# Optimization experiments

Measured on AMD Instinct MI355X. Metric: run time of the kernel, lower is better.

## Reference

```python
import jax, jax.numpy as jnp
import numpy as np

# dims: H heads, D=word_size (d_model), E=embed_dim per head, N=seq_len=n, K=linformer k
H, D, E, N, K = 16, 1024, 64, 4096, 256


def setup_inputs() -> dict:
    key = jax.random.key(0)
    ks = jax.random.split(key, 9)
    s = 0.02  # init scale for weights
    return {
        "x":  jax.random.normal(ks[0], (N, D), jnp.float32),
        # per-head QKV linears: torch Linear weight is (out=E, in=D), bias (E,)
        "Wq": jax.random.normal(ks[1], (H, E, D), jnp.float32) * s,
        "bq": jnp.zeros((H, E), jnp.float32),
        "Wk": jax.random.normal(ks[2], (H, E, D), jnp.float32) * s,
        "bk": jnp.zeros((H, E), jnp.float32),
        "Wv": jax.random.normal(ks[3], (H, E, D), jnp.float32) * s,
        "bv": jnp.zeros((H, E), jnp.float32),
        # per-head E/F sequence projections: Linear(n=N, k=K) -> weight (K, N), bias (K,)
        "Ew": jax.random.normal(ks[4], (H, K, N), jnp.float32) * s,
        "Eb": jnp.zeros((H, K), jnp.float32),
        "Fw": jax.random.normal(ks[5], (H, K, N), jnp.float32) * s,
        "Fb": jnp.zeros((H, K), jnp.float32),
        # output projection: Linear(H*E, E, bias=False) -> weight (E, H*E)
        "Wo": jax.random.normal(ks[6], (E, H * E), jnp.float32) * s,
    }


def reference(x, Wq, bq, Wk, bk, Wv, bv, Ew, Eb, Fw, Fb, Wo):
    # per-head Q/K/V projections, batched over heads: (H, N, E)
    q = jnp.einsum('nd,hed->hne', x, Wq) + bq[:, None, :]
    k = jnp.einsum('nd,hed->hne', x, Wk) + bk[:, None, :]
    v = jnp.einsum('nd,hed->hne', x, Wv) + bv[:, None, :]
    # low-rank sequence-length projection of K and V: (H, K, E)
    kp = jnp.einsum('hjn,hne->hje', Ew, k) + Eb[:, :, None]
    vp = jnp.einsum('hjn,hne->hje', Fw, v) + Fb[:, :, None]
    # scaled dot-product attention against projected keys: (H, N, K)
    score = jnp.einsum('hne,hje->hnj', q, kp) / jnp.sqrt(jnp.float32(E))
    attn = jax.nn.softmax(score, axis=-1)
    z = jnp.einsum('hnj,hje->hne', attn, vp)  # (H, N, E)
    # concat heads along feature dim (matches torch.cat(dim=1)): (N, H*E)
    zs = jnp.transpose(z, (1, 0, 2)).reshape(N, H * E)
    # final projection Linear(H*E, E, bias=False)
    return zs @ Wo.T  # (N, E)
```

## Files before the change

kernel.cpp:

```cpp
#include <hip/hip_runtime.h>
#include <hip/hip_bf16.h>

typedef __attribute__((ext_vector_type(4))) float f32x4;
typedef __attribute__((ext_vector_type(8))) short s16x8;
typedef __attribute__((ext_vector_type(4))) short s16x4;
typedef unsigned short u16;


__device__ __forceinline__ f32x4 mfma16(s16x8 a, s16x8 b, f32x4 c) {
    return __builtin_amdgcn_mfma_f32_16x16x32_bf16(a, b, c, 0, 0, 0);
}

__device__ __forceinline__ u16 bf(float f) {
    union { float f; unsigned u; } x; x.f = f;
    return (u16)((x.u + 0x7fffu + ((x.u >> 16) & 1u)) >> 16);
}
__device__ __forceinline__ unsigned pkbf(float a, float b) {
    union { float f; unsigned u; } x, y; x.f = a; y.f = b;
    unsigned ra = x.u + 0x7fffu + ((x.u >> 16) & 1u);
    unsigned rb = y.u + 0x7fffu + ((y.u >> 16) & 1u);
    return (ra >> 16) | (rb & 0xffff0000u);
}

__device__ __forceinline__ void gl_lds16(const u16* g, u16* l) {
    __builtin_amdgcn_global_load_lds(
        (const __attribute__((address_space(1))) unsigned*)g,
        (__attribute__((address_space(3))) unsigned*)l, 16, 0, 0);
}


__global__ __launch_bounds__(256) void cvt_all_kernel(
        const float* __restrict__ x,  const float* __restrict__ Wq,
        const float* __restrict__ Wk, const float* __restrict__ Wv,
        const float* __restrict__ Wo,
        u16* __restrict__ xb, u16* __restrict__ wb, u16* __restrict__ wob) {
    int i = blockIdx.x * 256 + threadIdx.x;
    const float* src; u16* dst; int off;
    if (i < 1048576)      { src = x;  dst = xb;            off = i; }
    else if (i < 1310720) { src = Wq; dst = wb;            off = i - 1048576; }
    else if (i < 1572864) { src = Wk; dst = wb + 1048576;  off = i - 1310720; }
    else if (i < 1835008) { src = Wv; dst = wb + 2097152;  off = i - 1572864; }
    else if (i < 1851392) { src = Wo; dst = wob;           off = i - 1835008; }
    else return;
    f32x4 v = ((const f32x4*)src)[off];
    union { s16x4 v; unsigned u[2]; } r;
    r.u[0] = pkbf(v.x, v.y);
    r.u[1] = pkbf(v.z, v.w);
    ((s16x4*)dst)[off] = r.v;
}


__global__ __launch_bounds__(256, 3) void qkv_kernel(
        const u16* __restrict__ xb, const u16* __restrict__ wb,
        const float* __restrict__ bq, const float* __restrict__ bk,
        const float* __restrict__ bv,
        u16* __restrict__ qo, u16* __restrict__ kTo, u16* __restrict__ vTo) {
    __shared__ u16 As[128 * 32];
    __shared__ u16 Bs[128 * 32];
    int bx   = blockIdx.x % 24;
    int by   = blockIdx.x / 24;
    int tid  = threadIdx.x;
    int lane = tid & 63, w = tid >> 6;
    int l15  = lane & 15, quad = lane >> 4;
    int wr   = w >> 1, wc = w & 1;

    const u16* Ag = xb + (size_t)(by * 128 + (tid >> 2)) * 1024 + (tid & 3) * 8;
    const u16* Bg = wb + (size_t)(bx * 128 + (tid >> 2)) * 1024 + (tid & 3) * 8;
    u16* Al = As + tid * 8;
    u16* Bl = Bs + tid * 8;

    const u16* abase = As + (wr * 64 + l15) * 32 + quad * 8;
    const u16* bbase = Bs + (wc * 64 + l15) * 32 + quad * 8;

    f32x4 acc[4][4] = {};
    for (int k0 = 0; k0 < 1024; k0 += 32) {
        gl_lds16(Ag + k0, Al);
        gl_lds16(Ag + 64 * 1024 + k0, Al + 64 * 32);
        gl_lds16(Bg + k0, Bl);
        gl_lds16(Bg + 64 * 1024 + k0, Bl + 64 * 32);
        __syncthreads();
        s16x8 a[4], b[4];
#pragma unroll
        for (int mi = 0; mi < 4; mi++) a[mi] = *(const s16x8*)(abase + mi * 16 * 32);
#pragma unroll
        for (int nj = 0; nj < 4; nj++) b[nj] = *(const s16x8*)(bbase + nj * 16 * 32);
#pragma unroll
        for (int mi = 0; mi < 4; mi++)
#pragma unroll
            for (int nj = 0; nj < 4; nj++) acc[mi][nj] = mfma16(a[mi], b[nj], acc[mi][nj]);
        __syncthreads();
    }

    int fblk = (bx * 128 + wc * 64) >> 6;
    int mat  = fblk >> 4, h = fblk & 15;
    const float* bias = (mat == 0) ? bq : (mat == 1 ? bk : bv);
#pragma unroll
    for (int nj = 0; nj < 4; nj++) {
        int e = nj * 16 + l15;
        float bb = bias[h * 64 + e];
#pragma unroll
        for (int mi = 0; mi < 4; mi++) {
            int n0 = by * 128 + wr * 64 + mi * 16 + quad * 4;
            f32x4 c = acc[mi][nj];
            if (mat == 0) {
                u16* p = qo + ((size_t)h * 4096 + n0) * 64 + e;
#pragma unroll
                for (int r = 0; r < 4; r++) p[(size_t)r * 64] = bf(c[r] + bb);
            } else {
                u16* p = (mat == 1 ? kTo : vTo) + ((size_t)h * 64 + e) * 4096 + n0;
                union { s16x4 v; u16 s[4]; } pk;
#pragma unroll
                for (int r = 0; r < 4; r++) pk.s[r] = bf(c[r] + bb);
                *(s16x4*)p = pk.v;
            }
        }
    }
}


__global__ __launch_bounds__(256, 2) void kpvp_kernel(
        const float* __restrict__ Ew, const float* __restrict__ Fw,
        const u16* __restrict__ kT, const u16* __restrict__ vT,
        float* __restrict__ accs) {
    __shared__ u16 As[256 * 40];
    __shared__ u16 Bs[64 * 32];
    int b    = blockIdx.x;
    int ks   = b & 15, h = (b >> 4) & 15, p = b >> 8;
    int tid  = threadIdx.x;
    int lane = tid & 63, w = tid >> 6;
    int l15  = lane & 15, quad = lane >> 4;

    const float* Ag = (p ? Fw : Ew)
        + (size_t)(h * 256 + (tid >> 3)) * 4096 + ks * 256 + (tid & 7) * 4;
    const u16* Bg = (p ? vT : kT)
        + ((size_t)h * 64 + (tid >> 2)) * 4096 + ks * 256 + (tid & 3) * 8;
    u16* Aw = As + (tid >> 3) * 40 + (tid & 7) * 4;
    u16* Bl = Bs + tid * 8;

    const u16* abase = As + (w * 64 + l15) * 40 + quad * 8;
    const u16* bbase = Bs + l15 * 32 + quad * 8;

    f32x4 acc[4][4] = {};
    for (int s = 0; s < 8; s++) {
        int kk = s * 32;
        gl_lds16(Bg + kk, Bl);
#pragma unroll
        for (int pr = 0; pr < 8; pr++) {
            f32x4 v = *(const f32x4*)(Ag + (size_t)pr * 32 * 4096 + kk);
            union { s16x4 q; unsigned u[2]; } rr;
            rr.u[0] = pkbf(v.x, v.y);
            rr.u[1] = pkbf(v.z, v.w);
            *(s16x4*)(Aw + pr * 32 * 40) = rr.q;
        }
        __syncthreads();
        s16x8 a[4], bb2[4];
#pragma unroll
        for (int mt = 0; mt < 4; mt++) a[mt] = *(const s16x8*)(abase + mt * 16 * 40);
#pragma unroll
        for (int nt = 0; nt < 4; nt++) bb2[nt] = *(const s16x8*)(bbase + nt * 16 * 32);
#pragma unroll
        for (int mt = 0; mt < 4; mt++)
#pragma unroll
            for (int nt = 0; nt < 4; nt++)
                acc[mt][nt] = mfma16(a[mt], bb2[nt], acc[mt][nt]);
        __syncthreads();
    }

    size_t base = (size_t)ks * 524288
        + ((size_t)(p * 16 + h) * 256 + w * 64 + quad * 4) * 64 + l15;
#pragma unroll
    for (int mt = 0; mt < 4; mt++)
#pragma unroll
        for (int nt = 0; nt < 4; nt++)
#pragma unroll
            for (int r = 0; r < 4; r++)
                accs[base + (size_t)(mt * 16 + r) * 64 + nt * 16] = acc[mt][nt][r];
}


__global__ __launch_bounds__(256) void packkv_kernel(
        const float* __restrict__ accs, const float* __restrict__ Eb,
        const float* __restrict__ Fb, u16* __restrict__ kp, u16* __restrict__ vpT) {
    int idx = blockIdx.x * 256 + threadIdx.x;
    float v = 0.f;
#pragma unroll
    for (int s = 0; s < 16; s++) v += accs[idx + (size_t)s * 524288];
    int p = idx >> 18, h = (idx >> 14) & 15, j = (idx >> 6) & 255, e = idx & 63;
    if (p == 0) {
        v += Eb[h * 256 + j];
        kp[((size_t)(h * 256 + j)) * 64 + e] = bf(v * 0.125f);
    } else {
        v += Fb[h * 256 + j];
        vpT[((size_t)(h * 64 + e)) * 256 + j] = bf(v);
    }
}


__global__ __launch_bounds__(256) void attn_kernel(
        const u16* __restrict__ q, const u16* __restrict__ kp,
        const u16* __restrict__ vpT, u16* __restrict__ zs) {
    __shared__ u16 ps[4][16][256];
    int bm   = blockIdx.x & 63, h = blockIdx.x >> 6;
    int lane = threadIdx.x & 63, w = threadIdx.x >> 6;
    int l15  = lane & 15, quad = lane >> 4;
    int nbase = bm * 64 + w * 16;

    f32x4 s[16] = {};
    const u16* qp  = q  + ((size_t)h * 4096 + nbase + l15) * 64 + quad * 8;
    const u16* kpp = kp + ((size_t)h * 256 + l15) * 64 + quad * 8;
#pragma unroll
    for (int e0 = 0; e0 < 64; e0 += 32) {
        s16x8 a = *(const s16x8*)(qp + e0);
#pragma unroll
        for (int jt = 0; jt < 16; jt++) {
            s16x8 b = *(const s16x8*)(kpp + jt * 16 * 64 + e0);
            s[jt] = mfma16(a, b, s[jt]);
        }
    }

    float lsum[4];
#pragma unroll
    for (int r = 0; r < 4; r++) {
        float m = s[0][r];
#pragma unroll
        for (int jt = 1; jt < 16; jt++) m = fmaxf(m, s[jt][r]);
        m = fmaxf(m, __shfl_xor(m, 1));
        m = fmaxf(m, __shfl_xor(m, 2));
        m = fmaxf(m, __shfl_xor(m, 4));
        m = fmaxf(m, __shfl_xor(m, 8));
        float l = 0.f;
#pragma unroll
        for (int jt = 0; jt < 16; jt++) {
            float pv = __expf(s[jt][r] - m);
            s[jt][r] = pv;
            l += pv;
        }
        l += __shfl_xor(l, 1);
        l += __shfl_xor(l, 2);
        l += __shfl_xor(l, 4);
        l += __shfl_xor(l, 8);
        lsum[r] = l;
    }

#pragma unroll
    for (int jt = 0; jt < 16; jt++)
#pragma unroll
        for (int r = 0; r < 4; r++)
            ps[w][quad * 4 + r][jt * 16 + l15] = bf(s[jt][r]);
    __syncthreads();

    f32x4 z[4] = {};
    const u16* vp = vpT + ((size_t)h * 64 + l15) * 256 + quad * 8;
#pragma unroll
    for (int kj = 0; kj < 8; kj++) {
        s16x8 a = *(const s16x8*)&ps[w][l15][kj * 32 + quad * 8];
#pragma unroll
        for (int et = 0; et < 4; et++) {
            s16x8 b = *(const s16x8*)(vp + et * 16 * 256 + kj * 32);
            z[et] = mfma16(a, b, z[et]);
        }
    }
#pragma unroll
    for (int et = 0; et < 4; et++) {
        int e = et * 16 + l15;
        u16* o = zs + ((size_t)(nbase + quad * 4)) * 1024 + h * 64 + e;
#pragma unroll
        for (int r = 0; r < 4; r++) o[(size_t)r * 1024] = bf(z[et][r] / lsum[r]);
    }
}


__global__ __launch_bounds__(256) void out_kernel(
        const u16* __restrict__ zs, const u16* __restrict__ wob,
        float* __restrict__ oslice) {
    int ks   = blockIdx.x & 3;
    int bm   = blockIdx.x >> 2;
    int lane = threadIdx.x & 63, w = threadIdx.x >> 6;
    int l15  = lane & 15, quad = lane >> 4;
    int row0 = bm * 128 + w * 32;

    const u16* A = zs  + (size_t)(row0 + l15) * 1024 + ks * 256 + quad * 8;
    const u16* B = wob + (size_t)l15 * 1024 + ks * 256 + quad * 8;

    f32x4 acc[2][4] = {};
    for (int k = 0; k < 256; k += 32) {
        s16x8 a0 = *(const s16x8*)(A + k);
        s16x8 a1 = *(const s16x8*)(A + 16 * 1024 + k);
#pragma unroll
        for (int nt = 0; nt < 4; nt++) {
            s16x8 bv = *(const s16x8*)(B + (size_t)nt * 16 * 1024 + k);
            acc[0][nt] = mfma16(a0, bv, acc[0][nt]);
            acc[1][nt] = mfma16(a1, bv, acc[1][nt]);
        }
    }
    float* os = oslice + (size_t)ks * 262144;
#pragma unroll
    for (int mt = 0; mt < 2; mt++)
#pragma unroll
        for (int nt = 0; nt < 4; nt++) {
            int e = nt * 16 + l15;
            int n0 = row0 + mt * 16 + quad * 4;
            float* o = os + (size_t)n0 * 64 + e;
#pragma unroll
            for (int r = 0; r < 4; r++) o[(size_t)r * 64] = acc[mt][nt][r];
        }
}

__global__ __launch_bounds__(256) void outred_kernel(
        const float* __restrict__ oslice, float* __restrict__ out) {
    int i = blockIdx.x * 256 + threadIdx.x;
    out[i] = oslice[i] + oslice[i + 262144] + oslice[i + 524288] + oslice[i + 786432];
}


extern "C" void kernel_launch(void* const* d_in, const int* in_sizes, int n_in,
                              void* d_out, int out_size, void* d_ws, size_t ws_size,
                              hipStream_t stream) {
    const float* x  = (const float*)d_in[0];
    const float* Wq = (const float*)d_in[1];
    const float* bq = (const float*)d_in[2];
    const float* Wk = (const float*)d_in[3];
    const float* bk = (const float*)d_in[4];
    const float* Wv = (const float*)d_in[5];
    const float* bv = (const float*)d_in[6];
    const float* Ew = (const float*)d_in[7];
    const float* Eb = (const float*)d_in[8];
    const float* Fw = (const float*)d_in[9];
    const float* Fb = (const float*)d_in[10];
    const float* Wo = (const float*)d_in[11];

    char* ws = (char*)d_ws;
    u16*   qb   = (u16*)(ws + 0);
    u16*   kT   = (u16*)(ws + 8388608);
    u16*   vT   = (u16*)(ws + 16777216);
    u16*   zsb  = (u16*)(ws + 25165824);
    float* accs = (float*)(ws + 33554432);
    u16*   kp   = (u16*)(ws + 67108864);
    u16*   vpT  = (u16*)(ws + 67633152);
    u16*   xb   = (u16*)(ws + 68157440);
    u16*   wb   = (u16*)(ws + 76546048);
    u16*   wob  = (u16*)(ws + 82837504);

    cvt_all_kernel<<<7232, 256, 0, stream>>>(x, Wq, Wk, Wv, Wo, xb, wb, wob);
    qkv_kernel<<<768, 256, 0, stream>>>(xb, wb, bq, bk, bv, qb, kT, vT);
    kpvp_kernel<<<512, 256, 0, stream>>>(Ew, Fw, kT, vT, accs);
    packkv_kernel<<<2048, 256, 0, stream>>>(accs, Eb, Fb, kp, vpT);
    attn_kernel<<<1024, 256, 0, stream>>>(qb, kp, vpT, zsb);
    out_kernel<<<128, 256, 0, stream>>>(zsb, wob, (float*)accs);
    outred_kernel<<<1024, 256, 0, stream>>>((const float*)accs, (float*)d_out);
}
```

Measured before the change: 300.4 us.

## Retile kpvp split-K and stage attention K/V projections in swizzled LDS

Measured after the change: 264.2 us. -12.0%, faster.

```diff
diff --git a/kernel.cpp b/kernel.cpp
--- a/kernel.cpp
+++ b/kernel.cpp
@@ -22,7 +22,7 @@
     return (ra >> 16) | (rb & 0xffff0000u);
 }
 
-__device__ __forceinline__ void gl_lds16(const u16* g, u16* l) {
+__device__ __forceinline__ void gl_lds16(const void* g, void* l) {
     __builtin_amdgcn_global_load_lds(
         (const __attribute__((address_space(1))) unsigned*)g,
         (__attribute__((address_space(3))) unsigned*)l, 16, 0, 0);
@@ -118,63 +118,79 @@
 }
 
 
-__global__ __launch_bounds__(256, 2) void kpvp_kernel(
+__global__ __launch_bounds__(512, 2) void kpvp_kernel(
         const float* __restrict__ Ew, const float* __restrict__ Fw,
         const u16* __restrict__ kT, const u16* __restrict__ vT,
         float* __restrict__ accs) {
-    __shared__ u16 As[256 * 40];
-    __shared__ u16 Bs[64 * 32];
-    int b    = blockIdx.x;
-    int ks   = b & 15, h = (b >> 4) & 15, p = b >> 8;
-    int tid  = threadIdx.x;
-    int lane = tid & 63, w = tid >> 6;
-    int l15  = lane & 15, quad = lane >> 4;
-
-    const float* Ag = (p ? Fw : Ew)
-        + (size_t)(h * 256 + (tid >> 3)) * 4096 + ks * 256 + (tid & 7) * 4;
-    const u16* Bg = (p ? vT : kT)
-        + ((size_t)h * 64 + (tid >> 2)) * 4096 + ks * 256 + (tid & 3) * 8;
-    u16* Aw = As + (tid >> 3) * 40 + (tid & 7) * 4;
-    u16* Bl = Bs + tid * 8;
-
-    const u16* abase = As + (w * 64 + l15) * 40 + quad * 8;
-    const u16* bbase = Bs + l15 * 32 + quad * 8;
-
-    f32x4 acc[4][4] = {};
+    __shared__ u16 Als[64 * 256];
+    __shared__ u16 Bls[64 * 256];
+    int b   = blockIdx.x;
+    int ks  = b & 1, jb = (b >> 1) & 3, h = (b >> 3) & 15, p = b >> 7;
+    int tid = threadIdx.x;
+    int w = tid >> 6, lane = tid & 63;
+    int l15 = lane & 15, quad = lane >> 4;
+    int wm = w >> 2, we = w & 3;
+
+    const float* Abase = (p ? Fw : Ew)
+        + (size_t)(h * 256 + jb * 64) * 4096 + ks * 2048;
+    const char* Bbase = (const char*)(p ? vT : kT)
+        + (size_t)h * 64 * 8192 + ks * 4096;
+
+    f32x4 areg[8];
+#pragma unroll
+    for (int pr = 0; pr < 8; pr++)
+        areg[pr] = *(const f32x4*)(Abase + (size_t)(pr * 8 + w) * 4096 + lane * 4);
+
+    f32x4 acc[2] = {};
+
+#pragma unroll
     for (int s = 0; s < 8; s++) {
-        int kk = s * 32;
-        gl_lds16(Bg + kk, Bl);
+        __syncthreads();
+#pragma unroll
+        for (int i = 0; i < 4; i++) {
+            int row = (w * 4 + i) * 2 + (lane >> 5);
+            int c   = lane & 31;
+            int cg  = (c & 24) | ((c & 7) ^ (row & 7));
+            gl_lds16(Bbase + (size_t)row * 8192 + s * 512 + cg * 16,
+                     (char*)Bls + (w * 4 + i) * 1024);
+        }
 #pragma unroll
         for (int pr = 0; pr < 8; pr++) {
-            f32x4 v = *(const f32x4*)(Ag + (size_t)pr * 32 * 4096 + kk);
+            int row = pr * 8 + w;
             union { s16x4 q; unsigned u[2]; } rr;
-            rr.u[0] = pkbf(v.x, v.y);
-            rr.u[1] = pkbf(v.z, v.w);
-            *(s16x4*)(Aw + pr * 32 * 40) = rr.q;
+            rr.u[0] = pkbf(areg[pr].x, areg[pr].y);
+            rr.u[1] = pkbf(areg[pr].z, areg[pr].w);
+            int c  = lane >> 1;
+            int cw = (c & 24) | ((c & 7) ^ (w & 7));
+            *(s16x4*)((char*)Als + row * 512 + cw * 16 + (lane & 1) * 8) = rr.q;
         }
         __syncthreads();
-        s16x8 a[4], bb2[4];
-#pragma unroll
-        for (int mt = 0; mt < 4; mt++) a[mt] = *(const s16x8*)(abase + mt * 16 * 40);
-#pragma unroll
-        for (int nt = 0; nt < 4; nt++) bb2[nt] = *(const s16x8*)(bbase + nt * 16 * 32);
-#pragma unroll
-        for (int mt = 0; mt < 4; mt++)
-#pragma unroll
-            for (int nt = 0; nt < 4; nt++)
-                acc[mt][nt] = mfma16(a[mt], bb2[nt], acc[mt][nt]);
-        __syncthreads();
-    }
-
-    size_t base = (size_t)ks * 524288
-        + ((size_t)(p * 16 + h) * 256 + w * 64 + quad * 4) * 64 + l15;
-#pragma unroll
-    for (int mt = 0; mt < 4; mt++)
-#pragma unroll
-        for (int nt = 0; nt < 4; nt++)
-#pragma unroll
-            for (int r = 0; r < 4; r++)
-                accs[base + (size_t)(mt * 16 + r) * 64 + nt * 16] = acc[mt][nt][r];
+        if (s < 7) {
+#pragma unroll
+            for (int pr = 0; pr < 8; pr++)
+                areg[pr] = *(const f32x4*)(Abase + (size_t)(pr * 8 + w) * 4096
+                                           + (s + 1) * 256 + lane * 4);
+        }
+#pragma unroll
+        for (int t = 0; t < 8; t++) {
+            int c  = 4 * t + quad;
+            int ca = (c & 24) | ((c & 7) ^ (l15 & 7));
+            s16x8 bv = *(const s16x8*)((char*)Bls + (we * 16 + l15) * 512 + ca * 16);
+            s16x8 a0 = *(const s16x8*)((char*)Als + (wm * 32 + l15) * 512 + ca * 16);
+            s16x8 a1 = *(const s16x8*)((char*)Als + (wm * 32 + 16 + l15) * 512 + ca * 16);
+            acc[0] = mfma16(a0, bv, acc[0]);
+            acc[1] = mfma16(a1, bv, acc[1]);
+        }
+    }
+
+    size_t obase = (size_t)ks * 524288 + ((size_t)(p * 16 + h) * 256 + jb * 64) * 64;
+#pragma unroll
+    for (int mt = 0; mt < 2; mt++)
+#pragma unroll
+        for (int r = 0; r < 4; r++) {
+            int jrow = wm * 32 + mt * 16 + quad * 4 + r;
+            accs[obase + (size_t)jrow * 64 + we * 16 + l15] = acc[mt][r];
+        }
 }
 
 
@@ -182,9 +198,7 @@
         const float* __restrict__ accs, const float* __restrict__ Eb,
         const float* __restrict__ Fb, u16* __restrict__ kp, u16* __restrict__ vpT) {
     int idx = blockIdx.x * 256 + threadIdx.x;
-    float v = 0.f;
-#pragma unroll
-    for (int s = 0; s < 16; s++) v += accs[idx + (size_t)s * 524288];
+    float v = accs[idx] + accs[idx + 524288];
     int p = idx >> 18, h = (idx >> 14) & 15, j = (idx >> 6) & 255, e = idx & 63;
     if (p == 0) {
         v += Eb[h * 256 + j];
@@ -196,26 +210,42 @@
 }
 
 
-__global__ __launch_bounds__(256) void attn_kernel(
+__global__ __launch_bounds__(256, 2) void attn_kernel(
         const u16* __restrict__ q, const u16* __restrict__ kp,
         const u16* __restrict__ vpT, u16* __restrict__ zs) {
+    __shared__ u16 kv[16384];
     __shared__ u16 ps[4][16][256];
     int bm   = blockIdx.x & 63, h = blockIdx.x >> 6;
-    int lane = threadIdx.x & 63, w = threadIdx.x >> 6;
+    int tid  = threadIdx.x;
+    int lane = tid & 63, w = tid >> 6;
     int l15  = lane & 15, quad = lane >> 4;
     int nbase = bm * 64 + w * 16;
 
+    {
+        int r8 = lane >> 3;
+        int cg = (lane & 7) ^ r8;
+        const u16* src = kp + (size_t)h * 16384;
+#pragma unroll
+        for (int it = 0; it < 8; it++) {
+            int row = it * 32 + w * 8 + r8;
+            gl_lds16(src + row * 64 + cg * 8, (char*)kv + it * 4096 + w * 1024);
+        }
+    }
+    const u16* qp = q + ((size_t)h * 4096 + nbase + l15) * 64 + quad * 8;
+    s16x8 qa0 = *(const s16x8*)(qp);
+    s16x8 qa1 = *(const s16x8*)(qp + 32);
+    __syncthreads();
+
     f32x4 s[16] = {};
-    const u16* qp  = q  + ((size_t)h * 4096 + nbase + l15) * 64 + quad * 8;
-    const u16* kpp = kp + ((size_t)h * 256 + l15) * 64 + quad * 8;
-#pragma unroll
-    for (int e0 = 0; e0 < 64; e0 += 32) {
-        s16x8 a = *(const s16x8*)(qp + e0);
-#pragma unroll
-        for (int jt = 0; jt < 16; jt++) {
-            s16x8 b = *(const s16x8*)(kpp + jt * 16 * 64 + e0);
-            s[jt] = mfma16(a, b, s[jt]);
-        }
+#pragma unroll
+    for (int jt = 0; jt < 16; jt++) {
+        int c0 = quad ^ (l15 & 7);
+        int c1 = (quad + 4) ^ (l15 & 7);
+        const char* rowp = (const char*)kv + (jt * 16 + l15) * 128;
+        s16x8 b0 = *(const s16x8*)(rowp + c0 * 16);
+        s16x8 b1 = *(const s16x8*)(rowp + c1 * 16);
+        s[jt] = mfma16(qa0, b0, s[jt]);
+        s[jt] = mfma16(qa1, b1, s[jt]);
     }
 
     float lsum[4];
@@ -242,22 +272,37 @@
         lsum[r] = l;
     }
 
+    __syncthreads();
+    {
+        int r2 = lane >> 5;
+        int c  = lane & 31;
+        const u16* src = vpT + (size_t)h * 16384;
+#pragma unroll
+        for (int it = 0; it < 8; it++) {
+            int row = it * 8 + w * 2 + r2;
+            int cg  = (c & 24) | ((c & 7) ^ (row & 7));
+            gl_lds16(src + row * 256 + cg * 8, (char*)kv + it * 4096 + w * 1024);
+        }
+    }
 #pragma unroll
     for (int jt = 0; jt < 16; jt++)
 #pragma unroll
-        for (int r = 0; r < 4; r++)
-            ps[w][quad * 4 + r][jt * 16 + l15] = bf(s[jt][r]);
+        for (int r = 0; r < 4; r++) {
+            int row = quad * 4 + r;
+            ps[w][row][(jt * 16 + l15) ^ ((row & 7) << 3)] = bf(s[jt][r]);
+        }
     __syncthreads();
 
     f32x4 z[4] = {};
-    const u16* vp = vpT + ((size_t)h * 64 + l15) * 256 + quad * 8;
 #pragma unroll
     for (int kj = 0; kj < 8; kj++) {
-        s16x8 a = *(const s16x8*)&ps[w][l15][kj * 32 + quad * 8];
+        s16x8 a = *(const s16x8*)&ps[w][l15][(kj * 32 + quad * 8) ^ ((l15 & 7) << 3)];
 #pragma unroll
         for (int et = 0; et < 4; et++) {
-            s16x8 b = *(const s16x8*)(vp + et * 16 * 256 + kj * 32);
-            z[et] = mfma16(a, b, z[et]);
+            int c  = kj * 4 + quad;
+            int cs = (c & 24) | ((c & 7) ^ (l15 & 7));
+            s16x8 bv = *(const s16x8*)((char*)kv + (et * 16 + l15) * 512 + cs * 16);
+            z[et] = mfma16(a, bv, z[et]);
         }
     }
 #pragma unroll
@@ -343,7 +388,7 @@
 
     cvt_all_kernel<<<7232, 256, 0, stream>>>(x, Wq, Wk, Wv, Wo, xb, wb, wob);
     qkv_kernel<<<768, 256, 0, stream>>>(xb, wb, bq, bk, bv, qb, kT, vT);
-    kpvp_kernel<<<512, 256, 0, stream>>>(Ew, Fw, kT, vT, accs);
+    kpvp_kernel<<<256, 512, 0, stream>>>(Ew, Fw, kT, vT, accs);
     packkv_kernel<<<2048, 256, 0, stream>>>(accs, Eb, Fb, kp, vpT);
     attn_kernel<<<1024, 256, 0, stream>>>(qb, kp, vpT, zsb);
     out_kernel<<<128, 256, 0, stream>>>(zsb, wob, (float*)accs);
```
